# Kernel tuning notes

Measured on AMD Instinct MI355X. Metric: run time of the kernel, lower is better.

Reference implementation:

```python
import jax, jax.numpy as jnp
import numpy as np

N_REUPLOADS = 3


def _qrun(x, Wp, bp, W1, b1, W2, b2):
    """Q-RUN layer: linear proj -> sin/cos reupload stack -> tiny per-channel MLP -> flatten.
    x: [..., in_dim]; Wp: [H2, in_dim]; W1: [mlp_h, 2*n_reuploads]; W2: [2, mlp_h].
    Returns [..., 2*H2].
    """
    p = jnp.einsum('...i,hi->...h', x, Wp) + bp                 # [..., H2]
    # features ordered [sin, cos, sin, cos, sin, cos] as in torch.stack of extend-ed list
    sc = jnp.stack([jnp.sin(p), jnp.cos(p)], axis=-1)           # [..., H2, 2]
    feats = jnp.tile(sc, (1,) * (sc.ndim - 1) + (N_REUPLOADS,))  # [..., H2, 6]
    h = jax.nn.relu(jnp.einsum('...k,mk->...m', feats, W1) + b1)  # [..., H2, 32]
    o = jnp.einsum('...m,om->...o', h, W2) + b2                 # [..., H2, 2]
    return o.reshape(o.shape[:-2] + (-1,))                      # flatten(start_dim=-2)


def setup_inputs() -> dict:
    key = jax.random.key(0)
    ks = jax.random.split(key, 20)
    H, I, MH, K = 5120, 27648, 32, 2 * N_REUPLOADS
    d = {}
    d['x'] = jax.random.normal(ks[0], (1, 256, H), dtype=jnp.float32)

    def mk(kbase, in_dim, out_half):
        k1, k2, k3, k4 = jax.random.split(kbase, 4)
        return (
            jax.random.normal(k1, (out_half, in_dim), jnp.float32) * (1.0 / np.sqrt(in_dim)),
            jnp.zeros((out_half,), jnp.float32),
            jax.random.normal(k2, (MH, K), jnp.float32) * 0.1,
            jnp.zeros((MH,), jnp.float32),
            jax.random.normal(k3, (2, MH), jnp.float32) * 0.01,
            jnp.zeros((2,), jnp.float32),
        )

    (d['Wg'], d['bg'], d['W1g'], d['b1g'], d['W2g'], d['b2g']) = mk(ks[1], H, I // 2)
    (d['Wu'], d['bu'], d['W1u'], d['b1u'], d['W2u'], d['b2u']) = mk(ks[2], H, I // 2)
    (d['Wd'], d['bd'], d['W1d'], d['b1d'], d['W2d'], d['b2d']) = mk(ks[3], I, H // 2)
    return d


def reference(x, Wg, bg, W1g, b1g, W2g, b2g,
              Wu, bu, W1u, b1u, W2u, b2u,
              Wd, bd, W1d, b1d, W2d, b2d):
    gate = _qrun(x, Wg, bg, W1g, b1g, W2g, b2g)   # [B,S,27648]
    up = _qrun(x, Wu, bu, W1u, b1u, W2u, b2u)     # [B,S,27648]
    h = jax.nn.silu(gate) * up
    return _qrun(h, Wd, bd, W1d, b1d, W2d, b2d)   # [B,S,5120]
```

## Files before the change

kernel.cpp:

```cpp
#include <hip/hip_runtime.h>
#include <stdint.h>

typedef unsigned short u16;
typedef __attribute__((ext_vector_type(8))) short short8;
typedef __attribute__((ext_vector_type(4))) float f32x4;

#define KGU  5120
#define NPD  2560
#define KD   27648
#define SPLITD 12
#define KCHD 2304
#define PEL (256*2560)

__device__ __forceinline__ uint32_t f2bf(float x) {
  uint32_t b = __float_as_uint(x);
  return (b + 0x7fffu + ((b >> 16) & 1u)) >> 16;
}
__device__ __forceinline__ uint32_t pk2(float lo, float hi) { return f2bf(lo) | (f2bf(hi) << 16); }
__device__ __forceinline__ uint32_t cvtpk(float lo, float hi) {
  uint32_t r;
  asm("v_cvt_pk_bf16_f32 %0, %1, %2" : "=v"(r) : "v"(lo), "v"(hi));
  return r;
}
__device__ __forceinline__ float silu(float x) {
  return x * __builtin_amdgcn_rcpf(1.f + __expf(-x));
}
#define MFMA16(a,b,c) __builtin_amdgcn_mfma_f32_16x16x32_bf16(a, b, c, 0, 0, 0)

__global__ __launch_bounds__(256) void k_cvt(const float* __restrict__ X, u16* __restrict__ XF) {
  const int kt = blockIdx.x;
  const int lane = threadIdx.x & 63, wv = threadIdx.x >> 6;
#pragma unroll
  for (int ii = 0; ii < 4; ++ii) {
    const int mt = wv * 4 + ii;
    const float* src = X + (size_t)(mt * 16 + (lane & 15)) * KGU + kt * 32 + (lane >> 4) * 8;
    float4 f0 = *(const float4*)src;
    float4 f1 = *(const float4*)(src + 4);
    uint4 v;
    v.x = cvtpk(f0.x, f0.y); v.y = cvtpk(f0.z, f0.w);
    v.z = cvtpk(f1.x, f1.y); v.w = cvtpk(f1.z, f1.w);
    *(uint4*)(XF + ((size_t)(kt * 16 + mt) * 64 + lane) * 8) = v;
  }
}

__global__ __launch_bounds__(1024, 6)
void k_gu(const u16* __restrict__ XF,
          const float* __restrict__ Wg, const float* __restrict__ bg,
          const float* __restrict__ W1g, const float* __restrict__ b1g,
          const float* __restrict__ W2g, const float* __restrict__ b2g,
          const float* __restrict__ Wu, const float* __restrict__ bu,
          const float* __restrict__ W1u, const float* __restrict__ b1u,
          const float* __restrict__ W2u, const float* __restrict__ b2u,
          u16* __restrict__ HF) {
  __shared__ __align__(16) char smem[32768 + 1536];
  const int tid = threadIdx.x, lane = tid & 63, wid = tid >> 6;
  const int s_ = lane & 15, quad = lane >> 4;
  const int bx = blockIdx.x;
  const int w = (bx & 7) * 54 + (bx >> 3);
  const int j0p = w * 32;

  float4* mc4 = (float4*)(smem + 32768);
  float*  mc1 = (float*)(smem + 32768 + 1024);
  if (tid < 64) {
    int sel = tid >> 5, m = tid & 31;
    const float* w1 = (sel ? W1u : W1g) + m * 6;
    const float* b1 = sel ? b1u : b1g;
    const float* w2 = sel ? W2u : W2g;
    mc4[sel * 32 + m] = make_float4(w1[0] + w1[2] + w1[4], w1[1] + w1[3] + w1[5], b1[m], w2[m]);
    mc1[sel * 32 + m] = w2[32 + m];
  }

  const int brow = tid >> 4, bk8 = tid & 15;
  const float* srcB = ((brow & 1) ? Wu : Wg) + (size_t)(j0p + (brow >> 1)) * KGU + bk8 * 8;
  const int bwr = ((tid >> 3) & 1) * 8192 + brow * 128 + (((tid & 7) ^ (brow & 7)) << 4);

  const short8* paB = (const short8*)XF + (size_t)wid * 64 + lane;

  f32x4 acc[4];
#pragma unroll
  for (int i = 0; i < 4; ++i) acc[i] = (f32x4)0.f;
  short8 A0, A1;
  float4 sA0, sA1, sB0, sB1;

  sA0 = *(const float4*)(srcB);       sA1 = *(const float4*)(srcB + 4);
  sB0 = *(const float4*)(srcB + 128); sB1 = *(const float4*)(srcB + 132);
  A0 = paB[0]; A1 = paB[1024];
  {
    uint4 v;
    v.x = cvtpk(sA0.x, sA0.y); v.y = cvtpk(sA0.z, sA0.w);
    v.z = cvtpk(sA1.x, sA1.y); v.w = cvtpk(sA1.z, sA1.w);
    *(uint4*)(smem + bwr) = v;
  }
  sA0 = *(const float4*)(srcB + 256); sA1 = *(const float4*)(srcB + 260);
  asm volatile("s_waitcnt lgkmcnt(0)" ::: "memory");
  __builtin_amdgcn_sched_barrier(0);
  __builtin_amdgcn_s_barrier();

  auto kkstep = [&](const char* bb, int gbase, short8& Au, int ktn) {
    const int g = ((gbase + quad) ^ (s_ & 7)) << 4;
    const char* p = bb + s_ * 128 + g;
    short8 b0 = *(const short8*)(p);
    short8 b1 = *(const short8*)(p + 2048);
    short8 b2 = *(const short8*)(p + 4096);
    short8 b3 = *(const short8*)(p + 6144);
    __builtin_amdgcn_s_setprio(1);
    acc[0] = MFMA16(Au, b0, acc[0]);
    acc[1] = MFMA16(Au, b1, acc[1]);
    acc[2] = MFMA16(Au, b2, acc[2]);
    acc[3] = MFMA16(Au, b3, acc[3]);
    __builtin_amdgcn_s_setprio(0);
    Au = paB[(size_t)ktn * 1024];
  };
  auto period = [&](int st, float4& W0, float4& W1) {
    const char* buf = smem + (st & 1) * 16384;
    const int base = st * 4;
    kkstep(buf,        0, A0, (base + 2 > 159) ? 159 : base + 2);
    kkstep(buf,        4, A1, (base + 3 > 159) ? 159 : base + 3);
    kkstep(buf + 8192, 0, A0, (base + 4 > 159) ? 159 : base + 4);
    kkstep(buf + 8192, 4, A1, (base + 5 > 159) ? 159 : base + 5);
    if (st < 39) {
      char* bufn = smem + ((st + 1) & 1) * 16384;
      uint4 v;
      v.x = cvtpk(W0.x, W0.y); v.y = cvtpk(W0.z, W0.w);
      v.z = cvtpk(W1.x, W1.y); v.w = cvtpk(W1.z, W1.w);
      *(uint4*)(bufn + bwr) = v;
      const int stf = (st + 3 > 39) ? 39 : st + 3;
      W0 = *(const float4*)(srcB + stf * 128);
      W1 = *(const float4*)(srcB + stf * 128 + 4);
      asm volatile("s_waitcnt lgkmcnt(0)" ::: "memory");
      __builtin_amdgcn_sched_barrier(0);
      __builtin_amdgcn_s_barrier();
    }
  };

#pragma unroll 1
  for (int sp = 0; sp < 20; ++sp) {
    period(2 * sp,     sB0, sB1);
    period(2 * sp + 1, sA0, sA1);
  }

  const int sel = lane & 1;
  const float b2v0 = sel ? b2u[0] : b2g[0];
  const float b2v1 = sel ? b2u[1] : b2g[1];
  const float4* mcs = mc4 + sel * 32;
  const float*  mcw = mc1 + sel * 32;
  char* HFb = (char*)HF;
#pragma unroll
  for (int ni = 0; ni < 4; ++ni) {
    const int c = ni * 16 + s_;
    const int j = j0p + (c >> 1);
    const float bp = sel ? bu[j] : bg[j];
    float sv[4], cv[4], o0[4], o1[4];
#pragma unroll
    for (int e = 0; e < 4; ++e) {
      float p = acc[ni][e] + bp;
      sv[e] = __sinf(p); cv[e] = __cosf(p);
      o0[e] = b2v0; o1[e] = b2v1;
    }
#pragma unroll 4
    for (int m = 0; m < 32; ++m) {
      float4 k4 = mcs[m]; float w2b = mcw[m];
#pragma unroll
      for (int e = 0; e < 4; ++e) {
        float hh = fmaxf(fmaf(sv[e], k4.x, fmaf(cv[e], k4.y, k4.z)), 0.f);
        o0[e] = fmaf(hh, k4.w, o0[e]);
        o1[e] = fmaf(hh, w2b, o1[e]);
      }
    }
#pragma unroll
    for (int e = 0; e < 4; ++e) {
      float t0 = __shfl_xor(o0[e], 1);
      float t1 = __shfl_xor(o1[e], 1);
      float g0 = sel ? t0 : o0[e];
      float u0 = sel ? o0[e] : t0;
      float g1 = sel ? t1 : o1[e];
      float u1 = sel ? o1[e] : t1;
      float h0 = silu(g0) * u0, h1 = silu(g1) * u1;
      if (!sel) {
        const int row = wid * 16 + quad * 4 + e;
        const int kt2 = j >> 4;
        const int lf2 = (row & 15) + 16 * ((j >> 2) & 3);
        *(uint32_t*)(HFb + ((size_t)(kt2 * 16 + wid) * 64 + lf2) * 16 + (j & 3) * 4)
            = pk2(h0, h1);
      }
    }
  }
}

__global__ __launch_bounds__(1024, 6)
void k_down(const u16* __restrict__ HF, const float* __restrict__ Wd, float* __restrict__ P2) {
  __shared__ __align__(16) char smem[32768];
  const int tid = threadIdx.x, lane = tid & 63, wid = tid >> 6;
  const int s_ = lane & 15, quad = lane >> 4;
  const int bx = blockIdx.x;
  const int w = (bx & 7) * 60 + (bx >> 3);
  const int sk = w / 40, nt = w - sk * 40;
  const int n0 = nt * 64;

  const int brow = tid >> 4, bk8 = tid & 15;
  const float* srcB = Wd + (size_t)(n0 + brow) * KD + sk * KCHD + bk8 * 8;
  const int bwr = ((tid >> 3) & 1) * 8192 + brow * 128 + (((tid & 7) ^ (brow & 7)) << 4);

  const short8* paB = (const short8*)HF + ((size_t)(sk * 72) * 16 + wid) * 64 + lane;

  f32x4 acc[4];
#pragma unroll
  for (int i = 0; i < 4; ++i) acc[i] = (f32x4)0.f;
  short8 A0, A1;
  float4 sA0, sA1, sB0, sB1;

  sA0 = *(const float4*)(srcB);       sA1 = *(const float4*)(srcB + 4);
  sB0 = *(const float4*)(srcB + 128); sB1 = *(const float4*)(srcB + 132);
  A0 = paB[0]; A1 = paB[1024];
  {
    uint4 v;
    v.x = cvtpk(sA0.x, sA0.y); v.y = cvtpk(sA0.z, sA0.w);
    v.z = cvtpk(sA1.x, sA1.y); v.w = cvtpk(sA1.z, sA1.w);
    *(uint4*)(smem + bwr) = v;
  }
  sA0 = *(const float4*)(srcB + 256); sA1 = *(const float4*)(srcB + 260);
  asm volatile("s_waitcnt lgkmcnt(0)" ::: "memory");
  __builtin_amdgcn_sched_barrier(0);
  __builtin_amdgcn_s_barrier();

  auto kkstep = [&](const char* bb, int gbase, short8& Au, int ktn) {
    const int g = ((gbase + quad) ^ (s_ & 7)) << 4;
    const char* p = bb + s_ * 128 + g;
    short8 b0 = *(const short8*)(p);
    short8 b1 = *(const short8*)(p + 2048);
    short8 b2 = *(const short8*)(p + 4096);
    short8 b3 = *(const short8*)(p + 6144);
    __builtin_amdgcn_s_setprio(1);
    acc[0] = MFMA16(Au, b0, acc[0]);
    acc[1] = MFMA16(Au, b1, acc[1]);
    acc[2] = MFMA16(Au, b2, acc[2]);
    acc[3] = MFMA16(Au, b3, acc[3]);
    __builtin_amdgcn_s_setprio(0);
    Au = paB[(size_t)ktn * 1024];
  };
  auto period = [&](int st, float4& W0, float4& W1) {
    const char* buf = smem + (st & 1) * 16384;
    const int base = st * 4;
    kkstep(buf,        0, A0, (base + 2 > 71) ? 71 : base + 2);
    kkstep(buf,        4, A1, (base + 3 > 71) ? 71 : base + 3);
    kkstep(buf + 8192, 0, A0, (base + 4 > 71) ? 71 : base + 4);
    kkstep(buf + 8192, 4, A1, (base + 5 > 71) ? 71 : base + 5);
    if (st < 17) {
      char* bufn = smem + ((st + 1) & 1) * 16384;
      uint4 v;
      v.x = cvtpk(W0.x, W0.y); v.y = cvtpk(W0.z, W0.w);
      v.z = cvtpk(W1.x, W1.y); v.w = cvtpk(W1.z, W1.w);
      *(uint4*)(bufn + bwr) = v;
      const int stf = (st + 3 > 17) ? 17 : st + 3;
      W0 = *(const float4*)(srcB + stf * 128);
      W1 = *(const float4*)(srcB + stf * 128 + 4);
      asm volatile("s_waitcnt lgkmcnt(0)" ::: "memory");
      __builtin_amdgcn_sched_barrier(0);
      __builtin_amdgcn_s_barrier();
    }
  };

#pragma unroll 1
  for (int sp = 0; sp < 9; ++sp) {
    period(2 * sp,     sB0, sB1);
    period(2 * sp + 1, sA0, sA1);
  }

  float* P = P2 + (size_t)sk * PEL;
#pragma unroll
  for (int ni = 0; ni < 4; ++ni) {
    const int n = n0 + ni * 16 + s_;
#pragma unroll
    for (int e = 0; e < 4; ++e)
      P[(size_t)(wid * 16 + quad * 4 + e) * NPD + n] = acc[ni][e];
  }
}

__global__ __launch_bounds__(256) void k_fin(const float* __restrict__ P2, const float* __restrict__ bd,
    const float* __restrict__ W1d, const float* __restrict__ b1d, const float* __restrict__ W2d,
    const float* __restrict__ b2d, float* __restrict__ out) {
  __shared__ float4 mc0[32];
  __shared__ float mc1[32];
  const int tid = threadIdx.x;
  if (tid < 32) {
    const float* w = W1d + tid * 6;
    mc0[tid] = make_float4(w[0] + w[2] + w[4], w[1] + w[3] + w[5], b1d[tid], W2d[tid]);
    mc1[tid] = W2d[32 + tid];
  }
  __syncthreads();
  const int idx = blockIdx.x * 256 + tid;
  const int m = idx / NPD, j = idx - m * NPD;
  float p = bd[j];
#pragma unroll
  for (int sk = 0; sk < SPLITD; ++sk) p += P2[(size_t)sk * PEL + idx];
  float s = __sinf(p), c = __cosf(p);
  float o0 = b2d[0], o1 = b2d[1];
#pragma unroll 4
  for (int mm = 0; mm < 32; ++mm) {
    float4 k = mc0[mm];
    float hh = fmaxf(fmaf(s, k.x, fmaf(c, k.y, k.z)), 0.f);
    o0 = fmaf(hh, k.w, o0);
    o1 = fmaf(hh, mc1[mm], o1);
  }
  *(float2*)&out[(size_t)m * 5120 + 2 * j] = make_float2(o0, o1);
}

extern "C" void kernel_launch(void* const* d_in, const int* in_sizes, int n_in,
                              void* d_out, int out_size, void* d_ws, size_t ws_size,
                              hipStream_t stream) {
  const float* x   = (const float*)d_in[0];
  const float* Wg  = (const float*)d_in[1];
  const float* bg  = (const float*)d_in[2];
  const float* W1g = (const float*)d_in[3];
  const float* b1g = (const float*)d_in[4];
  const float* W2g = (const float*)d_in[5];
  const float* b2g = (const float*)d_in[6];
  const float* Wu  = (const float*)d_in[7];
  const float* bu  = (const float*)d_in[8];
  const float* W1u = (const float*)d_in[9];
  const float* b1u = (const float*)d_in[10];
  const float* W2u = (const float*)d_in[11];
  const float* b2u = (const float*)d_in[12];
  const float* Wd  = (const float*)d_in[13];
  const float* bd  = (const float*)d_in[14];
  const float* W1d = (const float*)d_in[15];
  const float* b1d = (const float*)d_in[16];
  const float* W2d = (const float*)d_in[17];
  const float* b2d = (const float*)d_in[18];
  char* ws = (char*)d_ws;
  u16*  XF = (u16*)ws;
  u16*  HF = (u16*)(ws + 2621440);
  float* P2 = (float*)(ws + 16777216);
  if (ws_size < 48234496u) return;

  k_cvt<<<dim3(160), dim3(256), 0, stream>>>(x, XF);
  k_gu<<<dim3(432), dim3(1024), 0, stream>>>(XF, Wg, bg, W1g, b1g, W2g, b2g,
                                             Wu, bu, W1u, b1u, W2u, b2u, HF);
  k_down<<<dim3(480), dim3(1024), 0, stream>>>(HF, Wd, P2);
  k_fin<<<dim3(2560), dim3(256), 0, stream>>>(P2, bd, W1d, b1d, W2d, b2d, (float*)d_out);
}
```

Baseline: 315.9 us.

## Double K-tile depth per barrier stage with new LDS layout and deeper A prefetch

Both GEMM kernels now stage 256-wide K chunks (64 KB LDS double buffer) instead of 128-wide chunks, so each block runs half as many barrier periods. The LDS layout becomes one 4 KB slab per 32-K step with a 4-way XOR swizzle, and the A-operand register prefetch goes from two fragments ahead to four. The goal is to cut barrier and synchronisation overhead and keep more loads in flight per stage. In exchange LDS per block doubles and register pressure rises, which may lower occupancy.

```diff
diff --git a/kernel.cpp b/kernel.cpp
--- a/kernel.cpp
+++ b/kernel.cpp
@@ -52,15 +52,15 @@
           const float* __restrict__ W1u, const float* __restrict__ b1u,
           const float* __restrict__ W2u, const float* __restrict__ b2u,
           u16* __restrict__ HF) {
-  __shared__ __align__(16) char smem[32768 + 1536];
+  __shared__ __align__(16) char smem[65536 + 1536];
   const int tid = threadIdx.x, lane = tid & 63, wid = tid >> 6;
   const int s_ = lane & 15, quad = lane >> 4;
   const int bx = blockIdx.x;
   const int w = (bx & 7) * 54 + (bx >> 3);
   const int j0p = w * 32;
 
-  float4* mc4 = (float4*)(smem + 32768);
-  float*  mc1 = (float*)(smem + 32768 + 1024);
+  float4* mc4 = (float4*)(smem + 65536);
+  float*  mc1 = (float*)(smem + 65536 + 1024);
   if (tid < 64) {
     int sel = tid >> 5, m = tid & 31;
     const float* w1 = (sel ? W1u : W1g) + m * 6;
@@ -70,73 +70,73 @@
     mc1[sel * 32 + m] = w2[32 + m];
   }
 
-  const int brow = tid >> 4, bk8 = tid & 15;
-  const float* srcB = ((brow & 1) ? Wu : Wg) + (size_t)(j0p + (brow >> 1)) * KGU + bk8 * 8;
-  const int bwr = ((tid >> 3) & 1) * 8192 + brow * 128 + (((tid & 7) ^ (brow & 7)) << 4);
+  const int brow = tid >> 4, kc16 = tid & 15;
+  const float* srcB = ((brow & 1) ? Wu : Wg) + (size_t)(j0p + (brow >> 1)) * KGU + kc16 * 16;
+  const int kkb = kc16 >> 1, hh = kc16 & 1;
+  const int wadr0 = kkb * 4096 + brow * 64 + (((2 * hh)     ^ (brow & 3)) << 4);
+  const int wadr1 = kkb * 4096 + brow * 64 + (((2 * hh + 1) ^ (brow & 3)) << 4);
+  const int roff = s_ * 64 + ((quad ^ (s_ & 3)) << 4);
 
   const short8* paB = (const short8*)XF + (size_t)wid * 64 + lane;
 
   f32x4 acc[4];
 #pragma unroll
   for (int i = 0; i < 4; ++i) acc[i] = (f32x4)0.f;
-  short8 A0, A1;
-  float4 sA0, sA1, sB0, sB1;
-
-  sA0 = *(const float4*)(srcB);       sA1 = *(const float4*)(srcB + 4);
-  sB0 = *(const float4*)(srcB + 128); sB1 = *(const float4*)(srcB + 132);
-  A0 = paB[0]; A1 = paB[1024];
-  {
-    uint4 v;
-    v.x = cvtpk(sA0.x, sA0.y); v.y = cvtpk(sA0.z, sA0.w);
-    v.z = cvtpk(sA1.x, sA1.y); v.w = cvtpk(sA1.z, sA1.w);
-    *(uint4*)(smem + bwr) = v;
-  }
-  sA0 = *(const float4*)(srcB + 256); sA1 = *(const float4*)(srcB + 260);
+  short8 A[4];
+  float4 W[4];
+
+  auto loadW = [&](int st) {
+    const float* p = srcB + st * 256;
+    W[0] = *(const float4*)p;       W[1] = *(const float4*)(p + 4);
+    W[2] = *(const float4*)(p + 8); W[3] = *(const float4*)(p + 12);
+  };
+  auto stageW = [&](char* buf) {
+    uint4 v0, v1;
+    v0.x = cvtpk(W[0].x, W[0].y); v0.y = cvtpk(W[0].z, W[0].w);
+    v0.z = cvtpk(W[1].x, W[1].y); v0.w = cvtpk(W[1].z, W[1].w);
+    v1.x = cvtpk(W[2].x, W[2].y); v1.y = cvtpk(W[2].z, W[2].w);
+    v1.z = cvtpk(W[3].x, W[3].y); v1.w = cvtpk(W[3].z, W[3].w);
+    *(uint4*)(buf + wadr0) = v0;
+    *(uint4*)(buf + wadr1) = v1;
+  };
+
+  loadW(0);
+  A[0] = paB[0]; A[1] = paB[1024]; A[2] = paB[2048]; A[3] = paB[3072];
+  stageW(smem);
+  loadW(1);
   asm volatile("s_waitcnt lgkmcnt(0)" ::: "memory");
   __builtin_amdgcn_sched_barrier(0);
   __builtin_amdgcn_s_barrier();
 
-  auto kkstep = [&](const char* bb, int gbase, short8& Au, int ktn) {
-    const int g = ((gbase + quad) ^ (s_ & 7)) << 4;
-    const char* p = bb + s_ * 128 + g;
-    short8 b0 = *(const short8*)(p);
-    short8 b1 = *(const short8*)(p + 2048);
-    short8 b2 = *(const short8*)(p + 4096);
-    short8 b3 = *(const short8*)(p + 6144);
-    __builtin_amdgcn_s_setprio(1);
-    acc[0] = MFMA16(Au, b0, acc[0]);
-    acc[1] = MFMA16(Au, b1, acc[1]);
-    acc[2] = MFMA16(Au, b2, acc[2]);
-    acc[3] = MFMA16(Au, b3, acc[3]);
-    __builtin_amdgcn_s_setprio(0);
-    Au = paB[(size_t)ktn * 1024];
-  };
-  auto period = [&](int st, float4& W0, float4& W1) {
-    const char* buf = smem + (st & 1) * 16384;
-    const int base = st * 4;
-    kkstep(buf,        0, A0, (base + 2 > 159) ? 159 : base + 2);
-    kkstep(buf,        4, A1, (base + 3 > 159) ? 159 : base + 3);
-    kkstep(buf + 8192, 0, A0, (base + 4 > 159) ? 159 : base + 4);
-    kkstep(buf + 8192, 4, A1, (base + 5 > 159) ? 159 : base + 5);
-    if (st < 39) {
-      char* bufn = smem + ((st + 1) & 1) * 16384;
-      uint4 v;
-      v.x = cvtpk(W0.x, W0.y); v.y = cvtpk(W0.z, W0.w);
-      v.z = cvtpk(W1.x, W1.y); v.w = cvtpk(W1.z, W1.w);
-      *(uint4*)(bufn + bwr) = v;
-      const int stf = (st + 3 > 39) ? 39 : st + 3;
-      W0 = *(const float4*)(srcB + stf * 128);
-      W1 = *(const float4*)(srcB + stf * 128 + 4);
+#pragma unroll 1
+  for (int st = 0; st < 20; ++st) {
+    const char* buf = smem + (st & 1) * 32768;
+#pragma unroll
+    for (int kk = 0; kk < 8; ++kk) {
+      const char* p = buf + kk * 4096 + roff;
+      short8 b0 = *(const short8*)(p);
+      short8 b1 = *(const short8*)(p + 1024);
+      short8 b2 = *(const short8*)(p + 2048);
+      short8 b3 = *(const short8*)(p + 3072);
+      short8 Au = A[kk & 3];
+      __builtin_amdgcn_s_setprio(1);
+      acc[0] = MFMA16(Au, b0, acc[0]);
+      acc[1] = MFMA16(Au, b1, acc[1]);
+      acc[2] = MFMA16(Au, b2, acc[2]);
+      acc[3] = MFMA16(Au, b3, acc[3]);
+      __builtin_amdgcn_s_setprio(0);
+      int ktn = st * 8 + kk + 4; if (ktn > 159) ktn = 159;
+      A[kk & 3] = paB[(size_t)ktn * 1024];
+    }
+    if (st < 19) {
+      char* bufn = smem + ((st + 1) & 1) * 32768;
+      stageW(bufn);
+      int stf = st + 2; if (stf > 19) stf = 19;
+      loadW(stf);
       asm volatile("s_waitcnt lgkmcnt(0)" ::: "memory");
       __builtin_amdgcn_sched_barrier(0);
       __builtin_amdgcn_s_barrier();
     }
-  };
-
-#pragma unroll 1
-  for (int sp = 0; sp < 20; ++sp) {
-    period(2 * sp,     sB0, sB1);
-    period(2 * sp + 1, sA0, sA1);
   }
 
   const int sel = lane & 1;
@@ -162,9 +162,9 @@
       float4 k4 = mcs[m]; float w2b = mcw[m];
 #pragma unroll
       for (int e = 0; e < 4; ++e) {
-        float hh = fmaxf(fmaf(sv[e], k4.x, fmaf(cv[e], k4.y, k4.z)), 0.f);
-        o0[e] = fmaf(hh, k4.w, o0[e]);
-        o1[e] = fmaf(hh, w2b, o1[e]);
+        float hh2 = fmaxf(fmaf(sv[e], k4.x, fmaf(cv[e], k4.y, k4.z)), 0.f);
+        o0[e] = fmaf(hh2, k4.w, o0[e]);
+        o1[e] = fmaf(hh2, w2b, o1[e]);
       }
     }
 #pragma unroll
@@ -189,7 +189,7 @@
 
 __global__ __launch_bounds__(1024, 6)
 void k_down(const u16* __restrict__ HF, const float* __restrict__ Wd, float* __restrict__ P2) {
-  __shared__ __align__(16) char smem[32768];
+  __shared__ __align__(16) char smem[65536];
   const int tid = threadIdx.x, lane = tid & 63, wid = tid >> 6;
   const int s_ = lane & 15, quad = lane >> 4;
   const int bx = blockIdx.x;
@@ -197,73 +197,73 @@
   const int sk = w / 40, nt = w - sk * 40;
   const int n0 = nt * 64;
 
-  const int brow = tid >> 4, bk8 = tid & 15;
-  const float* srcB = Wd + (size_t)(n0 + brow) * KD + sk * KCHD + bk8 * 8;
-  const int bwr = ((tid >> 3) & 1) * 8192 + brow * 128 + (((tid & 7) ^ (brow & 7)) << 4);
+  const int brow = tid >> 4, kc16 = tid & 15;
+  const float* srcB = Wd + (size_t)(n0 + brow) * KD + sk * KCHD + kc16 * 16;
+  const int kkb = kc16 >> 1, hh = kc16 & 1;
+  const int wadr0 = kkb * 4096 + brow * 64 + (((2 * hh)     ^ (brow & 3)) << 4);
+  const int wadr1 = kkb * 4096 + brow * 64 + (((2 * hh + 1) ^ (brow & 3)) << 4);
+  const int roff = s_ * 64 + ((quad ^ (s_ & 3)) << 4);
 
   const short8* paB = (const short8*)HF + ((size_t)(sk * 72) * 16 + wid) * 64 + lane;
 
   f32x4 acc[4];
 #pragma unroll
   for (int i = 0; i < 4; ++i) acc[i] = (f32x4)0.f;
-  short8 A0, A1;
-  float4 sA0, sA1, sB0, sB1;
-
-  sA0 = *(const float4*)(srcB);       sA1 = *(const float4*)(srcB + 4);
-  sB0 = *(const float4*)(srcB + 128); sB1 = *(const float4*)(srcB + 132);
-  A0 = paB[0]; A1 = paB[1024];
-  {
-    uint4 v;
-    v.x = cvtpk(sA0.x, sA0.y); v.y = cvtpk(sA0.z, sA0.w);
-    v.z = cvtpk(sA1.x, sA1.y); v.w = cvtpk(sA1.z, sA1.w);
-    *(uint4*)(smem + bwr) = v;
-  }
-  sA0 = *(const float4*)(srcB + 256); sA1 = *(const float4*)(srcB + 260);
+  short8 A[4];
+  float4 W[4];
+
+  auto loadW = [&](int st) {
+    const float* p = srcB + st * 256;
+    W[0] = *(const float4*)p;       W[1] = *(const float4*)(p + 4);
+    W[2] = *(const float4*)(p + 8); W[3] = *(const float4*)(p + 12);
+  };
+  auto stageW = [&](char* buf) {
+    uint4 v0, v1;
+    v0.x = cvtpk(W[0].x, W[0].y); v0.y = cvtpk(W[0].z, W[0].w);
+    v0.z = cvtpk(W[1].x, W[1].y); v0.w = cvtpk(W[1].z, W[1].w);
+    v1.x = cvtpk(W[2].x, W[2].y); v1.y = cvtpk(W[2].z, W[2].w);
+    v1.z = cvtpk(W[3].x, W[3].y); v1.w = cvtpk(W[3].z, W[3].w);
+    *(uint4*)(buf + wadr0) = v0;
+    *(uint4*)(buf + wadr1) = v1;
+  };
+
+  loadW(0);
+  A[0] = paB[0]; A[1] = paB[1024]; A[2] = paB[2048]; A[3] = paB[3072];
+  stageW(smem);
+  loadW(1);
   asm volatile("s_waitcnt lgkmcnt(0)" ::: "memory");
   __builtin_amdgcn_sched_barrier(0);
   __builtin_amdgcn_s_barrier();
 
-  auto kkstep = [&](const char* bb, int gbase, short8& Au, int ktn) {
-    const int g = ((gbase + quad) ^ (s_ & 7)) << 4;
-    const char* p = bb + s_ * 128 + g;
-    short8 b0 = *(const short8*)(p);
-    short8 b1 = *(const short8*)(p + 2048);
-    short8 b2 = *(const short8*)(p + 4096);
-    short8 b3 = *(const short8*)(p + 6144);
-    __builtin_amdgcn_s_setprio(1);
-    acc[0] = MFMA16(Au, b0, acc[0]);
-    acc[1] = MFMA16(Au, b1, acc[1]);
-    acc[2] = MFMA16(Au, b2, acc[2]);
-    acc[3] = MFMA16(Au, b3, acc[3]);
-    __builtin_amdgcn_s_setprio(0);
-    Au = paB[(size_t)ktn * 1024];
-  };
-  auto period = [&](int st, float4& W0, float4& W1) {
-    const char* buf = smem + (st & 1) * 16384;
-    const int base = st * 4;
-    kkstep(buf,        0, A0, (base + 2 > 71) ? 71 : base + 2);
-    kkstep(buf,        4, A1, (base + 3 > 71) ? 71 : base + 3);
-    kkstep(buf + 8192, 0, A0, (base + 4 > 71) ? 71 : base + 4);
-    kkstep(buf + 8192, 4, A1, (base + 5 > 71) ? 71 : base + 5);
-    if (st < 17) {
-      char* bufn = smem + ((st + 1) & 1) * 16384;
-      uint4 v;
-      v.x = cvtpk(W0.x, W0.y); v.y = cvtpk(W0.z, W0.w);
-      v.z = cvtpk(W1.x, W1.y); v.w = cvtpk(W1.z, W1.w);
-      *(uint4*)(bufn + bwr) = v;
-      const int stf = (st + 3 > 17) ? 17 : st + 3;
-      W0 = *(const float4*)(srcB + stf * 128);
-      W1 = *(const float4*)(srcB + stf * 128 + 4);
+#pragma unroll 1
+  for (int st = 0; st < 9; ++st) {
+    const char* buf = smem + (st & 1) * 32768;
+#pragma unroll
+    for (int kk = 0; kk < 8; ++kk) {
+      const char* p = buf + kk * 4096 + roff;
+      short8 b0 = *(const short8*)(p);
+      short8 b1 = *(const short8*)(p + 1024);
+      short8 b2 = *(const short8*)(p + 2048);
+      short8 b3 = *(const short8*)(p + 3072);
+      short8 Au = A[kk & 3];
+      __builtin_amdgcn_s_setprio(1);
+      acc[0] = MFMA16(Au, b0, acc[0]);
+      acc[1] = MFMA16(Au, b1, acc[1]);
+      acc[2] = MFMA16(Au, b2, acc[2]);
+      acc[3] = MFMA16(Au, b3, acc[3]);
+      __builtin_amdgcn_s_setprio(0);
+      int ktn = st * 8 + kk + 4; if (ktn > 71) ktn = 71;
+      A[kk & 3] = paB[(size_t)ktn * 1024];
+    }
+    if (st < 8) {
+      char* bufn = smem + ((st + 1) & 1) * 32768;
+      stageW(bufn);
+      int stf = st + 2; if (stf > 8) stf = 8;
+      loadW(stf);
       asm volatile("s_waitcnt lgkmcnt(0)" ::: "memory");
       __builtin_amdgcn_sched_barrier(0);
       __builtin_amdgcn_s_barrier();
     }
-  };
-
-#pragma unroll 1
-  for (int sp = 0; sp < 9; ++sp) {
-    period(2 * sp,     sB0, sB1);
-    period(2 * sp + 1, sA0, sA1);
   }
 
   float* P = P2 + (size_t)sk * PEL;
```

Measured after the change: 317.0 us. About the same (+0.4%).
